# Optimization experiments

Measured on AMD Instinct MI355X. Metric: run time of the kernel, lower is better.

Reference implementation:

```python
import math
import jax, jax.numpy as jnp
import numpy as np

D_MODEL = 2048
HEAD = 128
DEPTH = 12
LAMBDA_INIT = 0.8 - 0.6 * math.exp(-0.3 * DEPTH)
RMS_EPS = float(np.finfo(np.float32).eps)  # torch RMSNorm default eps=None -> finfo.eps


def setup_inputs() -> dict:
    key = jax.random.key(0)
    ks = jax.random.split(key, 9)
    B, S = 2, 4096
    std_l = 0.1
    return {
        "x": jax.random.normal(ks[0], (B, S, D_MODEL), dtype=jnp.float32),
        "Wq": jax.random.normal(ks[1], (HEAD, D_MODEL), dtype=jnp.float32) / math.sqrt(D_MODEL),
        "Wk": jax.random.normal(ks[2], (HEAD, D_MODEL), dtype=jnp.float32) / math.sqrt(D_MODEL),
        "Wv": jax.random.normal(ks[3], (HEAD, D_MODEL), dtype=jnp.float32) / math.sqrt(D_MODEL),
        "lambda_q1": std_l * jax.random.normal(ks[4], (HEAD // 2,), dtype=jnp.float32),
        "lambda_q2": std_l * jax.random.normal(ks[5], (HEAD // 2,), dtype=jnp.float32),
        "lambda_k1": std_l * jax.random.normal(ks[6], (HEAD // 2,), dtype=jnp.float32),
        "lambda_k2": std_l * jax.random.normal(ks[7], (HEAD // 2,), dtype=jnp.float32),
        "rms_weight": jnp.ones((HEAD,), dtype=jnp.float32),
    }


def reference(x, Wq, Wk, Wv, lambda_q1, lambda_q2, lambda_k1, lambda_k2, rms_weight):
    # projections (torch Linear: x @ W.T)
    q = jnp.einsum("bsd,hd->bsh", x, Wq)
    k = jnp.einsum("bsd,hd->bsh", x, Wk)
    v = jnp.einsum("bsd,hd->bsh", x, Wv)
    h2 = HEAD // 2
    q1, q2 = q[..., :h2], q[..., h2:]
    k1, k2 = k[..., :h2], k[..., h2:]
    scale = 1.0 / math.sqrt(h2)
    attn1 = jax.nn.softmax(jnp.einsum("bqh,bkh->bqk", q1, k1) * scale, axis=-1)
    attn2 = jax.nn.softmax(jnp.einsum("bqh,bkh->bqk", q2, k2) * scale, axis=-1)
    lam = jnp.exp(jnp.dot(lambda_q1, lambda_k1)) - jnp.exp(jnp.dot(lambda_q2, lambda_k2)) + LAMBDA_INIT
    attn_out = jnp.einsum("bqk,bkh->bqh", attn1 - lam * attn2, v)
    # RMSNorm over last dim
    rms = jax.lax.rsqrt(jnp.mean(attn_out * attn_out, axis=-1, keepdims=True) + RMS_EPS)
    return (1.0 - LAMBDA_INIT) * (attn_out * rms * rms_weight)
```

## Files before the change

kernel.cpp:

```cpp
#include <hip/hip_runtime.h>
#include <hip/hip_bf16.h>
#include <math.h>

#define S_LEN 4096
#define DMODEL 2048
#define HEADD 128

typedef __attribute__((ext_vector_type(8))) short short8;
typedef __attribute__((ext_vector_type(4))) float floatx4;

__device__ __forceinline__ short f2bs(float f) {
  __hip_bfloat16 h = __float2bfloat16(f);
  short s; __builtin_memcpy(&s, &h, 2); return s;
}
__device__ __forceinline__ float bs2f(short s) {
  unsigned u = ((unsigned)(unsigned short)s) << 16;
  float f; __builtin_memcpy(&f, &u, 4); return f;
}
__device__ __forceinline__ int pkbf(float a, float b) {
  return (int)(((unsigned)(unsigned short)f2bs(b) << 16) |
               (unsigned)(unsigned short)f2bs(a));
}

__global__ __launch_bounds__(256) void convw_kernel(const float* __restrict__ wq,
                                                    const float* __restrict__ wk,
                                                    const float* __restrict__ wv,
                                                    short* __restrict__ wc) {
  const int per = 128 * 2048;
  int e = (blockIdx.x * blockDim.x + threadIdx.x) * 4;
  const float* src = (e < per) ? wq : (e < 2 * per) ? wk : wv;
  int off = e & (per - 1);
  float4 v = *(const float4*)(src + off);
  short4 r;
  r.x = f2bs(v.x); r.y = f2bs(v.y); r.z = f2bs(v.z); r.w = f2bs(v.w);
  *(short4*)(wc + e) = r;
}

__global__ __launch_bounds__(256, 4) void proj_kernel(const float* __restrict__ x,
                                                      const short* __restrict__ wc,
                                                      short* __restrict__ qa0,
                                                      short* __restrict__ qa1) {
  const int tid = threadIdx.x;
  const int w = tid >> 6;
  const int lane = tid & 63;
  const int lo = lane & 15, g = lane >> 4;
  const int id = blockIdx.x;
  const int mb = id & 255, nb = (id >> 8) & 1, kh = id >> 9;
  const int m0 = mb * 32;
  const int n0 = nb * 192;
  const int k0 = kh * 1024;
  short* qa = kh ? qa1 : qa0;

  __shared__ short xt[2][32][40];
  __shared__ short wt[2][192][40];

  const int xr = tid >> 3, xk = (tid & 7) * 4;
  const int wr = tid >> 2, wq4 = (tid & 3) * 8;
  const float* xsrc = x + (size_t)(m0 + xr) * DMODEL + k0 + xk;
  const short* wsrc = wc + (size_t)(n0 + wr) * DMODEL + k0 + wq4;

  const int mrow = (w >> 1) * 16;
  const int ncol = (w & 1) * 96;

  floatx4 acc[6];
#pragma unroll
  for (int t = 0; t < 6; ++t) acc[t] = floatx4{0.f, 0.f, 0.f, 0.f};

  {
    float4 xv = *(const float4*)(xsrc);
    short4 xs;
    xs.x = f2bs(xv.x); xs.y = f2bs(xv.y); xs.z = f2bs(xv.z); xs.w = f2bs(xv.w);
    *(short4*)(&xt[0][xr][xk]) = xs;
#pragma unroll
    for (int c = 0; c < 3; ++c) {
      int4 wv = *(const int4*)(wsrc + (size_t)c * 64 * DMODEL);
      *(int4*)(&wt[0][c * 64 + wr][wq4]) = wv;
    }
  }
  __syncthreads();

  int cur = 0;
#pragma unroll 1
  for (int it = 0; it < 32; ++it) {
    float4 xn;
    int4 wn0, wn1, wn2;
    if (it + 1 < 32) {
      const int kn = (it + 1) * 32;
      xn = *(const float4*)(xsrc + kn);
      wn0 = *(const int4*)(wsrc + kn);
      wn1 = *(const int4*)(wsrc + (size_t)64 * DMODEL + kn);
      wn2 = *(const int4*)(wsrc + (size_t)128 * DMODEL + kn);
    }

    short8 af = *(const short8*)(&xt[cur][mrow + lo][g * 8]);
#pragma unroll
    for (int t = 0; t < 6; ++t) {
      short8 bf = *(const short8*)(&wt[cur][ncol + t * 16 + lo][g * 8]);
      acc[t] = __builtin_amdgcn_mfma_f32_16x16x32_bf16(af, bf, acc[t], 0, 0, 0);
    }

    if (it + 1 < 32) {
      short4 xs;
      xs.x = f2bs(xn.x); xs.y = f2bs(xn.y); xs.z = f2bs(xn.z); xs.w = f2bs(xn.w);
      *(short4*)(&xt[cur ^ 1][xr][xk]) = xs;
      *(int4*)(&wt[cur ^ 1][0 * 64 + wr][wq4]) = wn0;
      *(int4*)(&wt[cur ^ 1][1 * 64 + wr][wq4]) = wn1;
      *(int4*)(&wt[cur ^ 1][2 * 64 + wr][wq4]) = wn2;
    }
    __syncthreads();
    cur ^= 1;
  }

#pragma unroll
  for (int t = 0; t < 6; ++t) {
    int n = n0 + ncol + t * 16 + lo;
#pragma unroll
    for (int j = 0; j < 4; ++j) {
      int m = m0 + mrow + g * 4 + j;
      qa[(size_t)m * 384 + n] = f2bs(acc[t][j]);
    }
  }
}

__global__ __launch_bounds__(256) void conv_qk_kernel(const short* __restrict__ qa0,
                                                      const short* __restrict__ qa1,
                                                      short* __restrict__ qm,
                                                      short* __restrict__ kb) {
  int e = (blockIdx.x * 256 + threadIdx.x) * 4;
  int m = e >> 8, c = e & 255;
  short4 a = *(const short4*)(qa0 + (size_t)m * 384 + c);
  short4 b = *(const short4*)(qa1 + (size_t)m * 384 + c);
  float vx = bs2f(a.x) + bs2f(b.x);
  float vy = bs2f(a.y) + bs2f(b.y);
  float vz = bs2f(a.z) + bs2f(b.z);
  float vw = bs2f(a.w) + bs2f(b.w);
  short4 r;
  if (c < 128) {
    r.x = f2bs(vx * 0.125f); r.y = f2bs(vy * 0.125f);
    r.z = f2bs(vz * 0.125f); r.w = f2bs(vw * 0.125f);
    *(short4*)(qm + (size_t)m * 128 + c) = r;
  } else {
    r.x = f2bs(vx); r.y = f2bs(vy); r.z = f2bs(vz); r.w = f2bs(vw);
    *(short4*)(kb + (size_t)m * 128 + (c - 128)) = r;
  }
}

__global__ __launch_bounds__(256) void conv_v_kernel(const short* __restrict__ qa0,
                                                     const short* __restrict__ qa1,
                                                     short* __restrict__ vt) {
  const int tid = threadIdx.x;
  const int bb = blockIdx.x >> 6, st = blockIdx.x & 63;
  const int s0 = st * 64;

  __shared__ short ld[64][136];

  const int r = tid >> 2, c8 = (tid & 3) * 32;
#pragma unroll
  for (int q = 0; q < 4; ++q) {
    const size_t off = (size_t)(bb * 4096 + s0 + r) * 384 + 256 + c8 + q * 8;
    short8 a = *(const short8*)(qa0 + off);
    short8 b = *(const short8*)(qa1 + off);
    short8 o;
#pragma unroll
    for (int i = 0; i < 8; ++i) o[i] = f2bs(bs2f(a[i]) + bs2f(b[i]));
    *(short8*)(&ld[r][c8 + q * 8]) = o;
  }
  __syncthreads();

  const int h = tid >> 1, sh = (tid & 1) * 32;
#pragma unroll
  for (int q = 0; q < 4; ++q) {
    short8 t;
#pragma unroll
    for (int i = 0; i < 8; ++i) t[i] = ld[sh + q * 8 + i][h];
    *(short8*)(vt + ((size_t)bb * 128 + h) * 4096 + s0 + sh + q * 8) = t;
  }
}

__global__ __launch_bounds__(256, 3) void attn_kernel(const short* __restrict__ qm,
                                                      const short* __restrict__ kb,
                                                      const short* __restrict__ vt,
                                                      short* __restrict__ po,
                                                      float* __restrict__ pls) {
  const int tid = threadIdx.x;
  const int w = tid >> 6;
  const int lane = tid & 63;
  const int lo = lane & 15, g = lane >> 4;
  const int qsp = w >> 1;
  const int s = w & 1;
  const int id = blockIdx.x;
  const int ksp = id & 7;
  const int qblk = id >> 3;
  const int b = qblk >> 6;
  const int kv_base = ksp * 512;

  __shared__ short kt[2][32 * 128];
  __shared__ short vl[2][128 * 32];

  const int kr0 = tid >> 4, kck = tid & 15;
  const int vr0 = tid >> 2, vck = tid & 3;
  const short* kS = kb + (size_t)b * S_LEN * HEADD;
  const short* vS = vt + (size_t)b * HEADD * S_LEN;
  const int kld0 = kr0 * 128 + ((kck ^ (kr0 & 7)) * 8);
  const int kld1 = (kr0 + 16) * 128 + ((kck ^ (kr0 & 7)) * 8);
  const int vld0 = vr0 * 32 + ((vck ^ (vr0 & 3)) * 8);
  const int vld1 = (vr0 + 64) * 32 + ((vck ^ (vr0 & 3)) * 8);

  const int rowqA = qblk * 64 + qsp * 32;
  const int rowqB = rowqA + 16;
  const short* qrowA = qm + (size_t)(rowqA + lo) * HEADD + s * 64;
  const short* qrowB = qm + (size_t)(rowqB + lo) * HEADD + s * 64;
  const short8 qA0 = *(const short8*)(qrowA + g * 8);
  const short8 qA1 = *(const short8*)(qrowA + 32 + g * 8);
  const short8 qB0 = *(const short8*)(qrowB + g * 8);
  const short8 qB1 = *(const short8*)(qrowB + 32 + g * 8);

  floatx4 accA[8], accB[8];
#pragma unroll
  for (int n = 0; n < 8; ++n) {
    accA[n] = floatx4{0.f, 0.f, 0.f, 0.f};
    accB[n] = floatx4{0.f, 0.f, 0.f, 0.f};
  }
  float lxA = 0.f, lxB = 0.f;

  const int kc0 = ((s * 8 + g) ^ (lo & 7)) * 8;
  const int kc1 = ((s * 8 + 4 + g) ^ (lo & 7)) * 8;
  const int kro0 = lo * 128, kro1 = (16 + lo) * 128;
  const int vco = (g ^ (lo & 3)) * 8;

  const int gA = (g & 1) * 2;
  const int idx0 = lo + 16 * gA, idx1 = idx0 + 16;
  const bool hi = (g >= 2);

  {
    int4 ka = *(const int4*)(kS + (size_t)(kv_base + kr0) * HEADD + kck * 8);
    int4 kbx = *(const int4*)(kS + (size_t)(kv_base + kr0 + 16) * HEADD + kck * 8);
    int4 va = *(const int4*)(vS + (size_t)vr0 * S_LEN + kv_base + vck * 8);
    int4 vb = *(const int4*)(vS + (size_t)(vr0 + 64) * S_LEN + kv_base + vck * 8);
    *(int4*)(&kt[0][kld0]) = ka;
    *(int4*)(&kt[0][kld1]) = kbx;
    *(int4*)(&vl[0][vld0]) = va;
    *(int4*)(&vl[0][vld1]) = vb;
  }
  __syncthreads();

  int cur = 0;
#pragma unroll 1
  for (int it = 0; it < 16; ++it) {
    int4 ka, kbx, va, vb;
    if (it + 1 < 16) {
      const int kvn = kv_base + (it + 1) * 32;
      ka  = *(const int4*)(kS + (size_t)(kvn + kr0) * HEADD + kck * 8);
      kbx = *(const int4*)(kS + (size_t)(kvn + kr0 + 16) * HEADD + kck * 8);
      va  = *(const int4*)(vS + (size_t)vr0 * S_LEN + kvn + vck * 8);
      vb  = *(const int4*)(vS + (size_t)(vr0 + 64) * S_LEN + kvn + vck * 8);
    }

    const short* kbase = &kt[cur][0];
    short8 a00 = *(const short8*)(kbase + kro0 + kc0);
    short8 a01 = *(const short8*)(kbase + kro0 + kc1);
    short8 a10 = *(const short8*)(kbase + kro1 + kc0);
    short8 a11 = *(const short8*)(kbase + kro1 + kc1);

    floatx4 z = floatx4{0.f, 0.f, 0.f, 0.f};
    floatx4 u;
    u = __builtin_amdgcn_mfma_f32_16x16x32_bf16(a00, qA0, z, 0, 0, 0);
    floatx4 T0A = __builtin_amdgcn_mfma_f32_16x16x32_bf16(a01, qA1, u, 0, 0, 0);
    u = __builtin_amdgcn_mfma_f32_16x16x32_bf16(a10, qA0, z, 0, 0, 0);
    floatx4 T1A = __builtin_amdgcn_mfma_f32_16x16x32_bf16(a11, qA1, u, 0, 0, 0);
    u = __builtin_amdgcn_mfma_f32_16x16x32_bf16(a00, qB0, z, 0, 0, 0);
    floatx4 T0B = __builtin_amdgcn_mfma_f32_16x16x32_bf16(a01, qB1, u, 0, 0, 0);
    u = __builtin_amdgcn_mfma_f32_16x16x32_bf16(a10, qB0, z, 0, 0, 0);
    floatx4 T1B = __builtin_amdgcn_mfma_f32_16x16x32_bf16(a11, qB1, u, 0, 0, 0);

    short8 paA, paB;
    {
      float p0 = __expf(T0A[0]), p1 = __expf(T0A[1]), p2 = __expf(T0A[2]), p3 = __expf(T0A[3]);
      float p4 = __expf(T1A[0]), p5 = __expf(T1A[1]), p6 = __expf(T1A[2]), p7 = __expf(T1A[3]);
      float lp = ((p0 + p1) + (p2 + p3)) + ((p4 + p5) + (p6 + p7));
      lp += __shfl_xor(lp, 16);
      lp += __shfl_xor(lp, 32);
      lxA += lp;
      int c00 = pkbf(p0, p1), c01 = pkbf(p2, p3);
      int c10 = pkbf(p4, p5), c11 = pkbf(p6, p7);
      int t0a = __shfl(c00, idx0), t0b = __shfl(c01, idx0);
      int t0c = __shfl(c00, idx1), t0d = __shfl(c01, idx1);
      int t1a = __shfl(c10, idx0), t1b = __shfl(c11, idx0);
      int t1c = __shfl(c10, idx1), t1d = __shfl(c11, idx1);
      int w0 = hi ? t1a : t0a, w1 = hi ? t1b : t0b;
      int w2 = hi ? t1c : t0c, w3 = hi ? t1d : t0d;
      int4 tmp = {w0, w1, w2, w3}; __builtin_memcpy(&paA, &tmp, 16);
    }
    {
      float p0 = __expf(T0B[0]), p1 = __expf(T0B[1]), p2 = __expf(T0B[2]), p3 = __expf(T0B[3]);
      float p4 = __expf(T1B[0]), p5 = __expf(T1B[1]), p6 = __expf(T1B[2]), p7 = __expf(T1B[3]);
      float lp = ((p0 + p1) + (p2 + p3)) + ((p4 + p5) + (p6 + p7));
      lp += __shfl_xor(lp, 16);
      lp += __shfl_xor(lp, 32);
      lxB += lp;
      int c00 = pkbf(p0, p1), c01 = pkbf(p2, p3);
      int c10 = pkbf(p4, p5), c11 = pkbf(p6, p7);
      int t0a = __shfl(c00, idx0), t0b = __shfl(c01, idx0);
      int t0c = __shfl(c00, idx1), t0d = __shfl(c01, idx1);
      int t1a = __shfl(c10, idx0), t1b = __shfl(c11, idx0);
      int t1c = __shfl(c10, idx1), t1d = __shfl(c11, idx1);
      int w0 = hi ? t1a : t0a, w1 = hi ? t1b : t0b;
      int w2 = hi ? t1c : t0c, w3 = hi ? t1d : t0d;
      int4 tmp = {w0, w1, w2, w3}; __builtin_memcpy(&paB, &tmp, 16);
    }

    const short* vbase = &vl[cur][0];
#pragma unroll
    for (int n = 0; n < 8; ++n) {
      short8 vf = *(const short8*)(vbase + (n * 16 + lo) * 32 + vco);
      accA[n] = __builtin_amdgcn_mfma_f32_16x16x32_bf16(paA, vf, accA[n], 0, 0, 0);
      accB[n] = __builtin_amdgcn_mfma_f32_16x16x32_bf16(paB, vf, accB[n], 0, 0, 0);
    }

    if (it + 1 < 16) {
      *(int4*)(&kt[cur ^ 1][kld0]) = ka;
      *(int4*)(&kt[cur ^ 1][kld1]) = kbx;
      *(int4*)(&vl[cur ^ 1][vld0]) = va;
      *(int4*)(&vl[cur ^ 1][vld1]) = vb;
    }
    __syncthreads();
    cur ^= 1;
  }

  short* pw = po + ((size_t)(ksp * 2 + s) * 8192) * 128;
#pragma unroll
  for (int j = 0; j < 4; ++j) {
    short8 pk;
#pragma unroll
    for (int n = 0; n < 8; ++n) pk[n] = f2bs(accA[n][j]);
    *(short8*)(pw + (size_t)(rowqA + g * 4 + j) * 128 + lo * 8) = pk;
#pragma unroll
    for (int n = 0; n < 8; ++n) pk[n] = f2bs(accB[n][j]);
    *(short8*)(pw + (size_t)(rowqB + g * 4 + j) * 128 + lo * 8) = pk;
  }
  if (g == 0) {
    pls[(size_t)(ksp * 2 + s) * 8192 + rowqA + lo] = lxA;
    pls[(size_t)(ksp * 2 + s) * 8192 + rowqB + lo] = lxB;
  }
}

__global__ __launch_bounds__(256) void merge_kernel(const short* __restrict__ po,
                                                    const float* __restrict__ pls,
                                                    const float* __restrict__ lq1,
                                                    const float* __restrict__ lq2,
                                                    const float* __restrict__ lk1,
                                                    const float* __restrict__ lk2,
                                                    const float* __restrict__ rmsw,
                                                    float* __restrict__ out) {
  const int tid = threadIdx.x;
  const int row = blockIdx.x * 16 + (tid >> 4);
  const int lo = tid & 15;

  float a1s = 0.f, a2s = 0.f;
  for (int i = 0; i < 64; ++i) {
    a1s = fmaf(lq1[i], lk1[i], a1s);
    a2s = fmaf(lq2[i], lk2[i], a2s);
  }
  const float lam = __expf(a1s) - __expf(a2s) + 0.7836057665316245f;

  float o1[8], o2[8];
#pragma unroll
  for (int n = 0; n < 8; ++n) { o1[n] = 0.f; o2[n] = 0.f; }
  float l1 = 0.f, l2 = 0.f;
#pragma unroll
  for (int ksp = 0; ksp < 8; ++ksp) {
    short8 sa = *(const short8*)(po + ((size_t)(ksp * 2 + 0) * 8192 + row) * 128 + lo * 8);
    short8 sb = *(const short8*)(po + ((size_t)(ksp * 2 + 1) * 8192 + row) * 128 + lo * 8);
#pragma unroll
    for (int n = 0; n < 8; ++n) { o1[n] += bs2f(sa[n]); o2[n] += bs2f(sb[n]); }
    l1 += pls[(size_t)(ksp * 2 + 0) * 8192 + row];
    l2 += pls[(size_t)(ksp * 2 + 1) * 8192 + row];
  }
  const float iL1 = 1.f / l1, iL2 = 1.f / l2;

  float v[8];
  float ssq = 0.f;
#pragma unroll
  for (int n = 0; n < 8; ++n) {
    v[n] = o1[n] * iL1 - lam * (o2[n] * iL2);
    ssq += v[n] * v[n];
  }
  ssq += __shfl_xor(ssq, 1);
  ssq += __shfl_xor(ssq, 2);
  ssq += __shfl_xor(ssq, 4);
  ssq += __shfl_xor(ssq, 8);
  const float rr = rsqrtf(ssq * (1.f / 128.f) + 1.1920928955078125e-07f);

  float* ob = out + (size_t)row * 128;
#pragma unroll
  for (int n = 0; n < 8; ++n) {
    int c = n * 16 + lo;
    ob[c] = 0.21639423346837554f * v[n] * rr * rmsw[c];
  }
}

extern "C" void kernel_launch(void* const* d_in, const int* in_sizes, int n_in,
                              void* d_out, int out_size, void* d_ws, size_t ws_size,
                              hipStream_t stream) {
  const float* x   = (const float*)d_in[0];
  const float* wq  = (const float*)d_in[1];
  const float* wk  = (const float*)d_in[2];
  const float* wv  = (const float*)d_in[3];
  const float* lq1 = (const float*)d_in[4];
  const float* lq2 = (const float*)d_in[5];
  const float* lk1 = (const float*)d_in[6];
  const float* lk2 = (const float*)d_in[7];
  const float* rw  = (const float*)d_in[8];
  float* out = (float*)d_out;

  char* ws = (char*)d_ws;
  short* qm  = (short*)(ws);
  short* kb  = (short*)(ws + (2u << 20));
  short* vt  = (short*)(ws + (4u << 20));
  short* wc  = (short*)(ws + (6u << 20));
  short* qa0 = (short*)(ws + (8u << 20));
  short* qa1 = (short*)(ws + (8u << 20) + 6291456u);
  short* po  = (short*)(ws + (8u << 20));
  float* pls = (float*)(ws + (40u << 20));

  convw_kernel<<<768, 256, 0, stream>>>(wq, wk, wv, wc);
  proj_kernel<<<1024, 256, 0, stream>>>(x, wc, qa0, qa1);
  conv_qk_kernel<<<2048, 256, 0, stream>>>(qa0, qa1, qm, kb);
  conv_v_kernel<<<128, 256, 0, stream>>>(qa0, qa1, vt);
  attn_kernel<<<1024, 256, 0, stream>>>(qm, kb, vt, po, pls);
  merge_kernel<<<512, 256, 0, stream>>>(po, pls, lq1, lq2, lk1, lk2, rw, out);
}
```

Measured before the change: 107.7 us.

## Drop split-K in projection, write Q/K/V directly, swizzle LDS tiles

```diff
diff --git a/kernel.cpp b/kernel.cpp
--- a/kernel.cpp
+++ b/kernel.cpp
@@ -36,79 +36,129 @@
   *(short4*)(wc + e) = r;
 }
 
-__global__ __launch_bounds__(256, 4) void proj_kernel(const float* __restrict__ x,
+__global__ __launch_bounds__(256, 3) void proj_kernel(const float* __restrict__ x,
                                                       const short* __restrict__ wc,
-                                                      short* __restrict__ qa0,
-                                                      short* __restrict__ qa1) {
+                                                      short* __restrict__ qm,
+                                                      short* __restrict__ kb,
+                                                      short* __restrict__ vstage) {
   const int tid = threadIdx.x;
   const int w = tid >> 6;
   const int lane = tid & 63;
   const int lo = lane & 15, g = lane >> 4;
   const int id = blockIdx.x;
-  const int mb = id & 255, nb = (id >> 8) & 1, kh = id >> 9;
+  const int nb = id >> 8, mb = id & 255;
   const int m0 = mb * 32;
   const int n0 = nb * 192;
-  const int k0 = kh * 1024;
-  short* qa = kh ? qa1 : qa0;
-
-  __shared__ short xt[2][32][40];
-  __shared__ short wt[2][192][40];
-
-  const int xr = tid >> 3, xk = (tid & 7) * 4;
-  const int wr = tid >> 2, wq4 = (tid & 3) * 8;
-  const float* xsrc = x + (size_t)(m0 + xr) * DMODEL + k0 + xk;
-  const short* wsrc = wc + (size_t)(n0 + wr) * DMODEL + k0 + wq4;
+
+  __shared__ short xt[2][16 * 64];
+  __shared__ short wt[2][96 * 64];
+
+  const int xr = tid >> 2, xc = tid & 3;
+  const bool doX = tid < 128;
+  const float* xsrc = x + (size_t)(m0 + (doX ? xr : 0)) * DMODEL + xc * 8;
+  const int xl = (xr >> 1) * 64 + ((((xr & 1) * 4 + xc) ^ ((xr >> 1) & 7)) * 8);
+  const int wr = tid >> 2, wq = tid & 3;
+  const short* wsrc = wc + (size_t)(n0 + wr) * DMODEL + wq * 8;
+  int wl0, wl1, wl2;
+  {
+    int R0 = wr, R1 = 64 + wr, R2 = 128 + wr;
+    wl0 = (R0 >> 1) * 64 + ((((R0 & 1) * 4 + wq) ^ ((R0 >> 1) & 7)) * 8);
+    wl1 = (R1 >> 1) * 64 + ((((R1 & 1) * 4 + wq) ^ ((R1 >> 1) & 7)) * 8);
+    wl2 = (R2 >> 1) * 64 + ((((R2 & 1) * 4 + wq) ^ ((R2 >> 1) & 7)) * 8);
+  }
 
   const int mrow = (w >> 1) * 16;
   const int ncol = (w & 1) * 96;
+  int aoff;
+  { int r = mrow + lo; aoff = (r >> 1) * 64 + ((((r & 1) * 4 + g) ^ ((r >> 1) & 7)) * 8); }
+  int boff[6];
+#pragma unroll
+  for (int t = 0; t < 6; ++t) {
+    int R = ncol + t * 16 + lo;
+    boff[t] = (R >> 1) * 64 + ((((R & 1) * 4 + g) ^ ((R >> 1) & 7)) * 8);
+  }
 
   floatx4 acc[6];
 #pragma unroll
   for (int t = 0; t < 6; ++t) acc[t] = floatx4{0.f, 0.f, 0.f, 0.f};
 
-  {
-    float4 xv = *(const float4*)(xsrc);
-    short4 xs;
-    xs.x = f2bs(xv.x); xs.y = f2bs(xv.y); xs.z = f2bs(xv.z); xs.w = f2bs(xv.w);
-    *(short4*)(&xt[0][xr][xk]) = xs;
-#pragma unroll
-    for (int c = 0; c < 3; ++c) {
-      int4 wv = *(const int4*)(wsrc + (size_t)c * 64 * DMODEL);
-      *(int4*)(&wt[0][c * 64 + wr][wq4]) = wv;
-    }
-  }
+  float4 xa0, xa1, xb0, xb1;
+  int4 wa0, wa1, wa2, wb0, wb1, wb2;
+
+  if (doX) { xa0 = *(const float4*)(xsrc); xa1 = *(const float4*)(xsrc + 4); }
+  wa0 = *(const int4*)(wsrc);
+  wa1 = *(const int4*)(wsrc + (size_t)64 * DMODEL);
+  wa2 = *(const int4*)(wsrc + (size_t)128 * DMODEL);
+  if (doX) {
+    short8 xs;
+    xs[0] = f2bs(xa0.x); xs[1] = f2bs(xa0.y); xs[2] = f2bs(xa0.z); xs[3] = f2bs(xa0.w);
+    xs[4] = f2bs(xa1.x); xs[5] = f2bs(xa1.y); xs[6] = f2bs(xa1.z); xs[7] = f2bs(xa1.w);
+    *(short8*)&xt[0][xl] = xs;
+  }
+  *(int4*)&wt[0][wl0] = wa0;
+  *(int4*)&wt[0][wl1] = wa1;
+  *(int4*)&wt[0][wl2] = wa2;
+  if (doX) { xb0 = *(const float4*)(xsrc + 32); xb1 = *(const float4*)(xsrc + 36); }
+  wb0 = *(const int4*)(wsrc + 32);
+  wb1 = *(const int4*)(wsrc + (size_t)64 * DMODEL + 32);
+  wb2 = *(const int4*)(wsrc + (size_t)128 * DMODEL + 32);
   __syncthreads();
 
-  int cur = 0;
 #pragma unroll 1
-  for (int it = 0; it < 32; ++it) {
-    float4 xn;
-    int4 wn0, wn1, wn2;
-    if (it + 1 < 32) {
-      const int kn = (it + 1) * 32;
-      xn = *(const float4*)(xsrc + kn);
-      wn0 = *(const int4*)(wsrc + kn);
-      wn1 = *(const int4*)(wsrc + (size_t)64 * DMODEL + kn);
-      wn2 = *(const int4*)(wsrc + (size_t)128 * DMODEL + kn);
-    }
-
-    short8 af = *(const short8*)(&xt[cur][mrow + lo][g * 8]);
-#pragma unroll
-    for (int t = 0; t < 6; ++t) {
-      short8 bf = *(const short8*)(&wt[cur][ncol + t * 16 + lo][g * 8]);
-      acc[t] = __builtin_amdgcn_mfma_f32_16x16x32_bf16(af, bf, acc[t], 0, 0, 0);
-    }
-
-    if (it + 1 < 32) {
-      short4 xs;
-      xs.x = f2bs(xn.x); xs.y = f2bs(xn.y); xs.z = f2bs(xn.z); xs.w = f2bs(xn.w);
-      *(short4*)(&xt[cur ^ 1][xr][xk]) = xs;
-      *(int4*)(&wt[cur ^ 1][0 * 64 + wr][wq4]) = wn0;
-      *(int4*)(&wt[cur ^ 1][1 * 64 + wr][wq4]) = wn1;
-      *(int4*)(&wt[cur ^ 1][2 * 64 + wr][wq4]) = wn2;
-    }
+  for (int it = 0; it < 64; it += 2) {
+    if (it + 2 < 64) {
+      const int k = (it + 2) * 32;
+      if (doX) { xa0 = *(const float4*)(xsrc + k); xa1 = *(const float4*)(xsrc + k + 4); }
+      wa0 = *(const int4*)(wsrc + k);
+      wa1 = *(const int4*)(wsrc + (size_t)64 * DMODEL + k);
+      wa2 = *(const int4*)(wsrc + (size_t)128 * DMODEL + k);
+    }
+    {
+      short8 af = *(const short8*)&xt[0][aoff];
+#pragma unroll
+      for (int t = 0; t < 6; ++t) {
+        short8 bf = *(const short8*)&wt[0][boff[t]];
+        acc[t] = __builtin_amdgcn_mfma_f32_16x16x32_bf16(af, bf, acc[t], 0, 0, 0);
+      }
+    }
+    if (doX) {
+      short8 xs;
+      xs[0] = f2bs(xb0.x); xs[1] = f2bs(xb0.y); xs[2] = f2bs(xb0.z); xs[3] = f2bs(xb0.w);
+      xs[4] = f2bs(xb1.x); xs[5] = f2bs(xb1.y); xs[6] = f2bs(xb1.z); xs[7] = f2bs(xb1.w);
+      *(short8*)&xt[1][xl] = xs;
+    }
+    *(int4*)&wt[1][wl0] = wb0;
+    *(int4*)&wt[1][wl1] = wb1;
+    *(int4*)&wt[1][wl2] = wb2;
     __syncthreads();
-    cur ^= 1;
+
+    if (it + 3 < 64) {
+      const int k = (it + 3) * 32;
+      if (doX) { xb0 = *(const float4*)(xsrc + k); xb1 = *(const float4*)(xsrc + k + 4); }
+      wb0 = *(const int4*)(wsrc + k);
+      wb1 = *(const int4*)(wsrc + (size_t)64 * DMODEL + k);
+      wb2 = *(const int4*)(wsrc + (size_t)128 * DMODEL + k);
+    }
+    {
+      short8 af = *(const short8*)&xt[1][aoff];
+#pragma unroll
+      for (int t = 0; t < 6; ++t) {
+        short8 bf = *(const short8*)&wt[1][boff[t]];
+        acc[t] = __builtin_amdgcn_mfma_f32_16x16x32_bf16(af, bf, acc[t], 0, 0, 0);
+      }
+    }
+    if (it + 2 < 64) {
+      if (doX) {
+        short8 xs;
+        xs[0] = f2bs(xa0.x); xs[1] = f2bs(xa0.y); xs[2] = f2bs(xa0.z); xs[3] = f2bs(xa0.w);
+        xs[4] = f2bs(xa1.x); xs[5] = f2bs(xa1.y); xs[6] = f2bs(xa1.z); xs[7] = f2bs(xa1.w);
+        *(short8*)&xt[0][xl] = xs;
+      }
+      *(int4*)&wt[0][wl0] = wa0;
+      *(int4*)&wt[0][wl1] = wa1;
+      *(int4*)&wt[0][wl2] = wa2;
+    }
+    __syncthreads();
   }
 
 #pragma unroll
@@ -117,36 +167,19 @@
 #pragma unroll
     for (int j = 0; j < 4; ++j) {
       int m = m0 + mrow + g * 4 + j;
-      qa[(size_t)m * 384 + n] = f2bs(acc[t][j]);
-    }
-  }
-}
-
-__global__ __launch_bounds__(256) void conv_qk_kernel(const short* __restrict__ qa0,
-                                                      const short* __restrict__ qa1,
-                                                      short* __restrict__ qm,
-                                                      short* __restrict__ kb) {
-  int e = (blockIdx.x * 256 + threadIdx.x) * 4;
-  int m = e >> 8, c = e & 255;
-  short4 a = *(const short4*)(qa0 + (size_t)m * 384 + c);
-  short4 b = *(const short4*)(qa1 + (size_t)m * 384 + c);
-  float vx = bs2f(a.x) + bs2f(b.x);
-  float vy = bs2f(a.y) + bs2f(b.y);
-  float vz = bs2f(a.z) + bs2f(b.z);
-  float vw = bs2f(a.w) + bs2f(b.w);
-  short4 r;
-  if (c < 128) {
-    r.x = f2bs(vx * 0.125f); r.y = f2bs(vy * 0.125f);
-    r.z = f2bs(vz * 0.125f); r.w = f2bs(vw * 0.125f);
-    *(short4*)(qm + (size_t)m * 128 + c) = r;
-  } else {
-    r.x = f2bs(vx); r.y = f2bs(vy); r.z = f2bs(vz); r.w = f2bs(vw);
-    *(short4*)(kb + (size_t)m * 128 + (c - 128)) = r;
-  }
-}
-
-__global__ __launch_bounds__(256) void conv_v_kernel(const short* __restrict__ qa0,
-                                                     const short* __restrict__ qa1,
+      float v = acc[t][j];
+      if (n < HEADD) {
+        qm[(size_t)m * HEADD + n] = f2bs(v * 0.125f);
+      } else if (n < 2 * HEADD) {
+        kb[(size_t)m * HEADD + (n - HEADD)] = f2bs(v);
+      } else {
+        vstage[(size_t)m * HEADD + (n - 2 * HEADD)] = f2bs(v);
+      }
+    }
+  }
+}
+
+__global__ __launch_bounds__(256) void conv_v_kernel(const short* __restrict__ vstage,
                                                      short* __restrict__ vt) {
   const int tid = threadIdx.x;
   const int bb = blockIdx.x >> 6, st = blockIdx.x & 63;
@@ -157,13 +190,8 @@
   const int r = tid >> 2, c8 = (tid & 3) * 32;
 #pragma unroll
   for (int q = 0; q < 4; ++q) {
-    const size_t off = (size_t)(bb * 4096 + s0 + r) * 384 + 256 + c8 + q * 8;
-    short8 a = *(const short8*)(qa0 + off);
-    short8 b = *(const short8*)(qa1 + off);
-    short8 o;
-#pragma unroll
-    for (int i = 0; i < 8; ++i) o[i] = f2bs(bs2f(a[i]) + bs2f(b[i]));
-    *(short8*)(&ld[r][c8 + q * 8]) = o;
+    const size_t off = (size_t)(bb * 4096 + s0 + r) * 128 + c8 + q * 8;
+    *(short8*)(&ld[r][c8 + q * 8]) = *(const short8*)(vstage + off);
   }
   __syncthreads();
 
@@ -418,15 +446,13 @@
   short* kb  = (short*)(ws + (2u << 20));
   short* vt  = (short*)(ws + (4u << 20));
   short* wc  = (short*)(ws + (6u << 20));
-  short* qa0 = (short*)(ws + (8u << 20));
-  short* qa1 = (short*)(ws + (8u << 20) + 6291456u);
+  short* vstage = (short*)(ws + (6u << 20) + 1572864u);
   short* po  = (short*)(ws + (8u << 20));
   float* pls = (float*)(ws + (40u << 20));
 
   convw_kernel<<<768, 256, 0, stream>>>(wq, wk, wv, wc);
-  proj_kernel<<<1024, 256, 0, stream>>>(x, wc, qa0, qa1);
-  conv_qk_kernel<<<2048, 256, 0, stream>>>(qa0, qa1, qm, kb);
-  conv_v_kernel<<<128, 256, 0, stream>>>(qa0, qa1, vt);
+  proj_kernel<<<512, 256, 0, stream>>>(x, wc, qm, kb, vstage);
+  conv_v_kernel<<<128, 256, 0, stream>>>(vstage, vt);
   attn_kernel<<<1024, 256, 0, stream>>>(qm, kb, vt, po, pls);
   merge_kernel<<<512, 256, 0, stream>>>(po, pls, lq1, lq2, lk1, lk2, rw, out);
 }
```

New measurement: 102.8 us. -4.5%, faster.
